# Kernel tuning notes

Measured on AMD Instinct MI355X. Metric: run time of the kernel, lower is better.

Reference implementation:

```python
import jax, jax.numpy as jnp
import numpy as np

B, S, D, N = 8, 2048, 1024, 1024
RMIN, RMAX = 0.9, 0.999
MAX_PHASE = 6.2831853
EPS = 1e-5


def _ln(v):
    # LayerNorm without affine params (elementwise_affine=False)
    mu = jnp.mean(v, axis=-1, keepdims=True)
    var = jnp.var(v, axis=-1, keepdims=True)
    return (v - mu) * jax.lax.rsqrt(var + EPS)


def setup_inputs() -> dict:
    key = jax.random.key(0)
    ks = jax.random.split(key, 12)
    x = jax.random.normal(ks[0], (B, S, D), dtype=jnp.float32)
    hidden_re = jnp.zeros((B, N), dtype=jnp.float32)
    hidden_im = jnp.zeros((B, N), dtype=jnp.float32)
    # LRU ring initialization (Orvieto et al. 2023)
    u1 = jax.random.uniform(ks[1], (N,), dtype=jnp.float32)
    u2 = jax.random.uniform(ks[2], (N,), dtype=jnp.float32)
    nu_log = jnp.log(-0.5 * jnp.log(u1 * (RMAX**2 - RMIN**2) + RMIN**2))
    theta_log = jnp.log(MAX_PHASE * u2)
    B_re = jax.random.normal(ks[3], (N, D), dtype=jnp.float32) / np.sqrt(2 * D)
    B_im = jax.random.normal(ks[4], (N, D), dtype=jnp.float32) / np.sqrt(2 * D)
    C_re = jax.random.normal(ks[5], (N, N), dtype=jnp.float32) / np.sqrt(N)
    C_im = jax.random.normal(ks[6], (N, N), dtype=jnp.float32) / np.sqrt(N)
    D_skip = jax.random.normal(ks[7], (N, D), dtype=jnp.float32) / np.sqrt(D)
    W_gate = jax.random.normal(ks[8], (N, D), dtype=jnp.float32) / np.sqrt(D)  # gating_proj
    W_con = jax.random.normal(ks[9], (D, N), dtype=jnp.float32) / np.sqrt(N)   # contract
    return {"x": x, "hidden_re": hidden_re, "hidden_im": hidden_im,
            "nu_log": nu_log, "theta_log": theta_log,
            "B_re": B_re, "B_im": B_im, "C_re": C_re, "C_im": C_im,
            "D_skip": D_skip, "W_gate": W_gate, "W_con": W_con}


def reference(x, hidden_re, hidden_im, nu_log, theta_log,
              B_re, B_im, C_re, C_im, D_skip, W_gate, W_con):
    residual = x
    # diagonal complex transition lambda and input normalizer gamma
    mag = jnp.exp(-jnp.exp(nu_log))                 # |lambda|, [N]
    phase = jnp.exp(theta_log)
    lam_re = mag * jnp.cos(phase)
    lam_im = mag * jnp.sin(phase)
    gamma = jnp.sqrt(1.0 - mag * mag)               # sqrt(1-|lambda|^2)
    # input projection (complex), pre-scaled by gamma: [B,S,N]
    u_re = jnp.einsum("bsd,nd->bsn", x, B_re) * gamma
    u_im = jnp.einsum("bsd,nd->bsn", x, B_im) * gamma
    # sequential linear recurrence h_t = lambda * h_{t-1} + u_t (complex)
    def step(h, u):
        h_re, h_im = h
        ur, ui = u
        nr = lam_re * h_re - lam_im * h_im + ur
        ni = lam_re * h_im + lam_im * h_re + ui
        return (nr, ni), (nr, ni)
    (hf_re, hf_im), (hs_re, hs_im) = jax.lax.scan(
        step, (hidden_re, hidden_im),
        (jnp.swapaxes(u_re, 0, 1), jnp.swapaxes(u_im, 0, 1)))  # time-major [S,B,N]
    hs_re = jnp.swapaxes(hs_re, 0, 1)  # [B,S,N]
    hs_im = jnp.swapaxes(hs_im, 0, 1)
    # y = Re(C h) + D x
    y = (jnp.einsum("bsn,mn->bsm", hs_re, C_re)
         - jnp.einsum("bsn,mn->bsm", hs_im, C_im)
         + jnp.einsum("bsd,md->bsm", x, D_skip))
    # gated norm / MLP fusion
    y = _ln(y)                                              # rnn_post_norm
    gate = jax.nn.gelu(_ln(jnp.einsum("bsd,nd->bsn", residual, W_gate)), approximate=False)
    y = y * gate
    y = jax.nn.gelu(_ln(y), approximate=False)              # contract_norm + activation
    out = jnp.einsum("bsn,dn->bsd", y, W_con)               # contract
    return (out, hf_re, hf_im)
```

## Files before the change

kernel.cpp:

```cpp
#include <hip/hip_runtime.h>
#include <math.h>

#define Bsz 8
#define Ssz 2048
#define Dsz 1024
#define Nsz 1024
#define CHUNKS 64
#define CLEN 32
#define Msz (Bsz * Ssz)

typedef unsigned short u16;
typedef __attribute__((ext_vector_type(8))) short short8;
typedef __attribute__((ext_vector_type(4))) float floatx4;

__device__ __forceinline__ float b2f(u16 u) {
    unsigned v = ((unsigned)u) << 16; float f; __builtin_memcpy(&f, &v, 4); return f;
}
__device__ __forceinline__ u16 f2b(float f) {
    unsigned u; __builtin_memcpy(&u, &f, 4);
    unsigned r = u + 0x7fffu + ((u >> 16) & 1u);
    return (u16)(r >> 16);
}

__global__ void cvt_kernel(const float* __restrict__ in, u16* __restrict__ out, int n4, float scale) {
    int i = blockIdx.x * blockDim.x + threadIdx.x;
    if (i < n4) {
        float4 v = ((const float4*)in)[i];
        ushort4 o;
        o.x = f2b(v.x * scale); o.y = f2b(v.y * scale);
        o.z = f2b(v.z * scale); o.w = f2b(v.w * scale);
        ((ushort4*)out)[i] = o;
    }
}

__global__ void lam_setup(const float* __restrict__ nu_log, const float* __restrict__ theta_log,
                          float* lam_re, float* lam_im, float* gam,
                          float* lamL_re, float* lamL_im) {
    int n = blockIdx.x * 256 + threadIdx.x;
    if (n >= Nsz) return;
    float mag = expf(-expf(nu_log[n]));
    float ph  = expf(theta_log[n]);
    float lr = mag * cosf(ph), li = mag * sinf(ph);
    lam_re[n] = lr; lam_im[n] = li;
    gam[n] = sqrtf(fmaxf(1.0f - mag * mag, 0.0f));
    float ar = lr, ai = li;
    #pragma unroll
    for (int i = 0; i < 5; ++i) { float nr = ar*ar - ai*ai; float ni = 2.0f*ar*ai; ar = nr; ai = ni; }
    lamL_re[n] = ar; lamL_im[n] = ai;
}

#define BM 128
#define BN 128
#define BK 32

struct GemmJob {
    const u16* A0; const u16* W0;
    const u16* A1; const u16* W1;
    const u16* A2; const u16* W2;
    int P;
    float* outF;
    u16*   outB;
    const float* colscale;
};
struct GemmBatch { GemmJob j[3]; };

__global__ __launch_bounds__(256, 2)
void gemm_bt(GemmBatch batch, int M, int N, int K) {
    const GemmJob job = batch.j[blockIdx.z];
    __shared__ u16 As[BM * BK];
    __shared__ u16 Ws[BN * BK];
    const int tid  = threadIdx.x;
    const int wave = tid >> 6, lane = tid & 63;
    const int bm = blockIdx.x, bn = blockIdx.y;
    const int wm = (wave >> 1) * 64, wn = (wave & 1) * 64;

    floatx4 acc[4][4];
    #pragma unroll
    for (int i = 0; i < 4; ++i)
        #pragma unroll
        for (int j = 0; j < 4; ++j) acc[i][j] = (floatx4){0.f, 0.f, 0.f, 0.f};

    const u16* Aps[3] = { job.A0, job.A1, job.A2 };
    const u16* Wps[3] = { job.W0, job.W1, job.W2 };

    const int srow = wave * 32 + (lane >> 2);
    const int scol = (((lane & 3) ^ ((lane >> 3) & 3))) * 8;
    const int frow = lane & 15;
    const int fk   = (((lane >> 4) ^ ((frow >> 1) & 3))) * 8;

    for (int p = 0; p < job.P; ++p) {
        const u16* A = Aps[p];
        const u16* W = Wps[p];
        const u16* gAb = A + (size_t)(bm * BM + srow) * K + scol;
        const u16* gWb = W + (size_t)(bn * BN + srow) * K + scol;
        for (int kk = 0; kk < K; kk += BK) {
            __syncthreads();
            #pragma unroll
            for (int jj = 0; jj < 2; ++jj) {
                const u16* gA = gAb + (size_t)(jj * 16) * K + kk;
                const u16* gW = gWb + (size_t)(jj * 16) * K + kk;
                u16* lA = As + (wave * 32 + jj * 16) * BK;
                u16* lW = Ws + (wave * 32 + jj * 16) * BK;
                __builtin_amdgcn_global_load_lds((const __attribute__((address_space(1))) void*)gA,
                                                 (__attribute__((address_space(3))) void*)lA, 16, 0, 0);
                __builtin_amdgcn_global_load_lds((const __attribute__((address_space(1))) void*)gW,
                                                 (__attribute__((address_space(3))) void*)lW, 16, 0, 0);
            }
            __syncthreads();
            short8 af[4], wf[4];
            #pragma unroll
            for (int i = 0; i < 4; ++i)
                af[i] = *(const short8*)(As + (wm + i * 16 + frow) * BK + fk);
            #pragma unroll
            for (int i = 0; i < 4; ++i)
                wf[i] = *(const short8*)(Ws + (wn + i * 16 + frow) * BK + fk);
            #pragma unroll
            for (int mi = 0; mi < 4; ++mi)
                #pragma unroll
                for (int ni = 0; ni < 4; ++ni)
                    acc[mi][ni] = __builtin_amdgcn_mfma_f32_16x16x32_bf16(af[mi], wf[ni], acc[mi][ni], 0, 0, 0);
        }
    }

    const int rgrp = lane >> 4;
    const int ccol = lane & 15;
    #pragma unroll
    for (int mi = 0; mi < 4; ++mi) {
        #pragma unroll
        for (int r = 0; r < 4; ++r) {
            int row = bm * BM + wm + mi * 16 + rgrp * 4 + r;
            #pragma unroll
            for (int ni = 0; ni < 4; ++ni) {
                int col = bn * BN + wn + ni * 16 + ccol;
                float v = acc[mi][ni][r];
                if (job.colscale) v *= job.colscale[col];
                size_t idx = (size_t)row * N + col;
                if (job.outF) job.outF[idx] = v;
                else          job.outB[idx] = f2b(v);
            }
        }
    }
}

__global__ void scan_phase1(const u16* __restrict__ u_re, const u16* __restrict__ u_im,
                            const float* __restrict__ lam_re, const float* __restrict__ lam_im,
                            float* __restrict__ carry_re, float* __restrict__ carry_im) {
    int n = blockIdx.x * 256 + threadIdx.x;
    int c = blockIdx.y, b = blockIdx.z;
    float lr = lam_re[n], li = lam_im[n];
    size_t base = ((size_t)b * Ssz + (size_t)c * CLEN) * Nsz + n;
    float hr = 0.f, hi = 0.f;
    #pragma unroll
    for (int t = 0; t < CLEN; ++t) {
        float ur = b2f(u_re[base + (size_t)t * Nsz]);
        float ui = b2f(u_im[base + (size_t)t * Nsz]);
        float nr = fmaf(lr, hr, fmaf(-li, hi, ur));
        float ni = fmaf(lr, hi, fmaf( li, hr, ui));
        hr = nr; hi = ni;
    }
    size_t ci = ((size_t)b * CHUNKS + c) * Nsz + n;
    carry_re[ci] = hr; carry_im[ci] = hi;
}

__global__ void scan_phase2(const float* __restrict__ carry_re, const float* __restrict__ carry_im,
                            const float* __restrict__ lamL_re, const float* __restrict__ lamL_im,
                            const float* __restrict__ hid_re, const float* __restrict__ hid_im,
                            float* __restrict__ entry_re, float* __restrict__ entry_im,
                            float* __restrict__ out_base) {
    int n = blockIdx.x * 256 + threadIdx.x;
    int b = blockIdx.y;
    float Lr = lamL_re[n], Li = lamL_im[n];
    float Hr = hid_re[b * Nsz + n], Hi = hid_im[b * Nsz + n];
    for (int c = 0; c < CHUNKS; ++c) {
        size_t ci = ((size_t)b * CHUNKS + c) * Nsz + n;
        entry_re[ci] = Hr; entry_im[ci] = Hi;
        float cr = carry_re[ci], cim = carry_im[ci];
        float nr = fmaf(Lr, Hr, fmaf(-Li, Hi, cr));
        float ni = fmaf(Lr, Hi, fmaf( Li, Hr, cim));
        Hr = nr; Hi = ni;
    }
    out_base[(size_t)16777216 + (size_t)b * Nsz + n] = Hr;
    out_base[(size_t)16777216 + 8192 + (size_t)b * Nsz + n] = Hi;
}

__global__ void scan_phase3(const u16* __restrict__ u_re, const u16* __restrict__ u_im,
                            const float* __restrict__ lam_re, const float* __restrict__ lam_im,
                            const float* __restrict__ entry_re, const float* __restrict__ entry_im,
                            u16* __restrict__ hs_re, u16* __restrict__ hs_im) {
    int n = blockIdx.x * 256 + threadIdx.x;
    int c = blockIdx.y, b = blockIdx.z;
    float lr = lam_re[n], li = lam_im[n];
    size_t ci = ((size_t)b * CHUNKS + c) * Nsz + n;
    float hr = entry_re[ci], hi = entry_im[ci];
    size_t base = ((size_t)b * Ssz + (size_t)c * CLEN) * Nsz + n;
    #pragma unroll
    for (int t = 0; t < CLEN; ++t) {
        float ur = b2f(u_re[base + (size_t)t * Nsz]);
        float ui = b2f(u_im[base + (size_t)t * Nsz]);
        float nr = fmaf(lr, hr, fmaf(-li, hi, ur));
        float ni = fmaf(lr, hi, fmaf( li, hr, ui));
        hr = nr; hi = ni;
        hs_re[base + (size_t)t * Nsz] = f2b(hr);
        hs_im[base + (size_t)t * Nsz] = f2b(hi);
    }
}

__device__ __forceinline__ float waveReduce(float v) {
    #pragma unroll
    for (int off = 32; off > 0; off >>= 1) v += __shfl_down(v, off, 64);
    return v;
}
__device__ __forceinline__ float gelu_exact(float x) {
    return 0.5f * x * (1.0f + erff(x * 0.70710678118654752f));
}

__global__ __launch_bounds__(256)
void fuse_ln(const u16* __restrict__ y_raw, const u16* __restrict__ gate_pre, u16* __restrict__ y3) {
    int row = blockIdx.x;
    int tid = threadIdx.x;
    int wave = tid >> 6, lane = tid & 63;
    size_t base = (size_t)row * Nsz + tid * 4;
    ushort4 yv = *(const ushort4*)(y_raw + base);
    ushort4 gv = *(const ushort4*)(gate_pre + base);
    float y[4] = { b2f(yv.x), b2f(yv.y), b2f(yv.z), b2f(yv.w) };
    float g[4] = { b2f(gv.x), b2f(gv.y), b2f(gv.z), b2f(gv.w) };

    float sy = 0.f, sy2 = 0.f, sg = 0.f, sg2 = 0.f;
    #pragma unroll
    for (int i = 0; i < 4; ++i) {
        sy += y[i]; sy2 += y[i] * y[i];
        sg += g[i]; sg2 += g[i] * g[i];
    }
    __shared__ float sh[16];
    sy = waveReduce(sy); sy2 = waveReduce(sy2);
    sg = waveReduce(sg); sg2 = waveReduce(sg2);
    if (lane == 0) { sh[wave] = sy; sh[wave + 4] = sy2; sh[wave + 8] = sg; sh[wave + 12] = sg2; }
    __syncthreads();
    sy  = sh[0] + sh[1] + sh[2] + sh[3];
    sy2 = sh[4] + sh[5] + sh[6] + sh[7];
    sg  = sh[8] + sh[9] + sh[10] + sh[11];
    sg2 = sh[12] + sh[13] + sh[14] + sh[15];
    const float inv = 1.0f / (float)Nsz;
    float muy = sy * inv, vary = sy2 * inv - muy * muy, ry = rsqrtf(vary + 1e-5f);
    float mug = sg * inv, varg = sg2 * inv - mug * mug, rg = rsqrtf(varg + 1e-5f);

    float y2[4]; float s2 = 0.f, s22 = 0.f;
    #pragma unroll
    for (int i = 0; i < 4; ++i) {
        float ly = (y[i] - muy) * ry;
        float lg = (g[i] - mug) * rg;
        float t = ly * gelu_exact(lg);
        y2[i] = t; s2 += t; s22 += t * t;
    }
    s2 = waveReduce(s2); s22 = waveReduce(s22);
    __syncthreads();
    if (lane == 0) { sh[wave] = s2; sh[wave + 4] = s22; }
    __syncthreads();
    s2  = sh[0] + sh[1] + sh[2] + sh[3];
    s22 = sh[4] + sh[5] + sh[6] + sh[7];
    float mu2 = s2 * inv, var2 = s22 * inv - mu2 * mu2, r2 = rsqrtf(var2 + 1e-5f);
    ushort4 ov;
    ov.x = f2b(gelu_exact((y2[0] - mu2) * r2));
    ov.y = f2b(gelu_exact((y2[1] - mu2) * r2));
    ov.z = f2b(gelu_exact((y2[2] - mu2) * r2));
    ov.w = f2b(gelu_exact((y2[3] - mu2) * r2));
    *(ushort4*)(y3 + base) = ov;
}

extern "C" void kernel_launch(void* const* d_in, const int* in_sizes, int n_in,
                              void* d_out, int out_size, void* d_ws, size_t ws_size,
                              hipStream_t stream) {
    const float* x         = (const float*)d_in[0];
    const float* hid_re    = (const float*)d_in[1];
    const float* hid_im    = (const float*)d_in[2];
    const float* nu_log    = (const float*)d_in[3];
    const float* theta_log = (const float*)d_in[4];
    const float* B_re      = (const float*)d_in[5];
    const float* B_im      = (const float*)d_in[6];
    const float* C_re      = (const float*)d_in[7];
    const float* C_im      = (const float*)d_in[8];
    const float* D_skip    = (const float*)d_in[9];
    const float* W_gate    = (const float*)d_in[10];
    const float* W_con     = (const float*)d_in[11];
    float* out = (float*)d_out;

    char* ws = (char*)d_ws;
    const size_t MB = 1ull << 20;
    u16* wBre  = (u16*)(ws + 0 * MB);
    u16* wBim  = (u16*)(ws + 2 * MB);
    u16* wCre  = (u16*)(ws + 4 * MB);
    u16* wCimN = (u16*)(ws + 6 * MB);
    u16* wDsk  = (u16*)(ws + 8 * MB);
    u16* wWg   = (u16*)(ws + 10 * MB);
    u16* wWc   = (u16*)(ws + 12 * MB);
    float* lam_re = (float*)(ws + 14 * MB);
    float* lam_im = lam_re + 1024;
    float* gam    = lam_re + 2048;
    float* lamLre = lam_re + 3072;
    float* lamLim = lam_re + 4096;
    u16* xb    = (u16*)(ws + 16 * MB);
    u16* u_re  = (u16*)(ws + 48 * MB);
    u16* u_im  = (u16*)(ws + 80 * MB);
    u16* gate  = (u16*)(ws + 112 * MB);
    u16* hs_re = (u16*)(ws + 144 * MB);
    u16* hs_im = (u16*)(ws + 176 * MB);
    float* carry_re = (float*)(ws + 208 * MB);
    float* carry_im = (float*)(ws + 210 * MB);
    float* entry_re = (float*)(ws + 212 * MB);
    float* entry_im = (float*)(ws + 214 * MB);
    u16* y_raw = u_re;
    u16* y3    = u_im;

    cvt_kernel<<<16384, 256, 0, stream>>>(x, xb, (Msz * Dsz) / 4, 1.0f);
    cvt_kernel<<<1024, 256, 0, stream>>>(B_re,   wBre,  (Nsz * Dsz) / 4, 1.0f);
    cvt_kernel<<<1024, 256, 0, stream>>>(B_im,   wBim,  (Nsz * Dsz) / 4, 1.0f);
    cvt_kernel<<<1024, 256, 0, stream>>>(C_re,   wCre,  (Nsz * Nsz) / 4, 1.0f);
    cvt_kernel<<<1024, 256, 0, stream>>>(C_im,   wCimN, (Nsz * Nsz) / 4, -1.0f);
    cvt_kernel<<<1024, 256, 0, stream>>>(D_skip, wDsk,  (Nsz * Dsz) / 4, 1.0f);
    cvt_kernel<<<1024, 256, 0, stream>>>(W_gate, wWg,   (Nsz * Dsz) / 4, 1.0f);
    cvt_kernel<<<1024, 256, 0, stream>>>(W_con,  wWc,   (Dsz * Nsz) / 4, 1.0f);
    lam_setup<<<4, 256, 0, stream>>>(nu_log, theta_log, lam_re, lam_im, gam, lamLre, lamLim);

    GemmBatch b1 = {};
    b1.j[0] = { xb, wBre, nullptr, nullptr, nullptr, nullptr, 1, nullptr, u_re, gam };
    b1.j[1] = { xb, wBim, nullptr, nullptr, nullptr, nullptr, 1, nullptr, u_im, gam };
    b1.j[2] = { xb, wWg,  nullptr, nullptr, nullptr, nullptr, 1, nullptr, gate, nullptr };
    gemm_bt<<<dim3(Msz / BM, Nsz / BN, 3), 256, 0, stream>>>(b1, Msz, Nsz, Dsz);

    scan_phase1<<<dim3(Nsz / 256, CHUNKS, Bsz), 256, 0, stream>>>(u_re, u_im, lam_re, lam_im, carry_re, carry_im);
    scan_phase2<<<dim3(Nsz / 256, Bsz), 256, 0, stream>>>(carry_re, carry_im, lamLre, lamLim,
                                                          hid_re, hid_im, entry_re, entry_im, out);
    scan_phase3<<<dim3(Nsz / 256, CHUNKS, Bsz), 256, 0, stream>>>(u_re, u_im, lam_re, lam_im,
                                                                  entry_re, entry_im, hs_re, hs_im);

    GemmBatch b2 = {};
    b2.j[0] = { hs_re, wCre, hs_im, wCimN, xb, wDsk, 3, nullptr, y_raw, nullptr };
    gemm_bt<<<dim3(Msz / BM, Nsz / BN, 1), 256, 0, stream>>>(b2, Msz, Nsz, Nsz);

    fuse_ln<<<Msz, 256, 0, stream>>>(y_raw, gate, y3);

    GemmBatch b3 = {};
    b3.j[0] = { y3, wWc, nullptr, nullptr, nullptr, nullptr, 1, out, nullptr, nullptr };
    gemm_bt<<<dim3(Msz / BM, Dsz / BN, 1), 256, 0, stream>>>(b3, Msz, Dsz, Nsz);

    (void)in_sizes; (void)n_in; (void)out_size; (void)ws_size;
}
```

Measured before the change: 527.7 us.

## Double GEMM K-tile to 64 with new LDS swizzle and batch conversions

Raises the GEMM K tile from 32 to 64 and reworks the global-to-LDS load pattern and XOR swizzle to match, so each barrier pair now covers two MFMA sub-steps. This halves the number of synchronisations and loop iterations per K sweep. Shared memory per block doubles, which may limit how many blocks fit per CU. Separately, the eight fp32-to-bf16 conversion launches are merged into one kernel that picks its job from a block-offset table, removing launch overhead.

```diff
diff --git a/kernel.cpp b/kernel.cpp
--- a/kernel.cpp
+++ b/kernel.cpp
@@ -22,14 +22,28 @@
     return (u16)(r >> 16);
 }
 
-__global__ void cvt_kernel(const float* __restrict__ in, u16* __restrict__ out, int n4, float scale) {
-    int i = blockIdx.x * blockDim.x + threadIdx.x;
-    if (i < n4) {
-        float4 v = ((const float4*)in)[i];
+struct CvtJobs {
+    const float* src[8];
+    u16* dst[8];
+    int n4[8];
+    float scale[8];
+    int blk_start[9];
+};
+
+__global__ __launch_bounds__(256)
+void cvt_multi(CvtJobs J) {
+    int b = blockIdx.x;
+    int j = 0;
+    #pragma unroll
+    for (int t = 0; t < 7; ++t) if (b >= J.blk_start[t + 1]) j = t + 1;
+    int i = (b - J.blk_start[j]) * 256 + threadIdx.x;
+    if (i < J.n4[j]) {
+        float4 v = ((const float4*)J.src[j])[i];
+        float s = J.scale[j];
         ushort4 o;
-        o.x = f2b(v.x * scale); o.y = f2b(v.y * scale);
-        o.z = f2b(v.z * scale); o.w = f2b(v.w * scale);
-        ((ushort4*)out)[i] = o;
+        o.x = f2b(v.x * s); o.y = f2b(v.y * s);
+        o.z = f2b(v.z * s); o.w = f2b(v.w * s);
+        ((ushort4*)J.dst[j])[i] = o;
     }
 }
 
@@ -51,7 +65,7 @@
 
 #define BM 128
 #define BN 128
-#define BK 32
+#define BK 64
 
 struct GemmJob {
     const u16* A0; const u16* W0;
@@ -83,42 +97,48 @@
     const u16* Aps[3] = { job.A0, job.A1, job.A2 };
     const u16* Wps[3] = { job.W0, job.W1, job.W2 };
 
-    const int srow = wave * 32 + (lane >> 2);
-    const int scol = (((lane & 3) ^ ((lane >> 3) & 3))) * 8;
+    const int srow8 = lane >> 3;
+    const int scol  = ((lane & 7) ^ srow8) * 8;
     const int frow = lane & 15;
-    const int fk   = (((lane >> 4) ^ ((frow >> 1) & 3))) * 8;
+    const int fq   = lane >> 4;
+    const int fsw  = frow & 7;
 
     for (int p = 0; p < job.P; ++p) {
         const u16* A = Aps[p];
         const u16* W = Wps[p];
-        const u16* gAb = A + (size_t)(bm * BM + srow) * K + scol;
-        const u16* gWb = W + (size_t)(bn * BN + srow) * K + scol;
+        const u16* gAb = A + (size_t)(bm * BM + srow8) * K + scol;
+        const u16* gWb = W + (size_t)(bn * BN + srow8) * K + scol;
         for (int kk = 0; kk < K; kk += BK) {
             __syncthreads();
             #pragma unroll
-            for (int jj = 0; jj < 2; ++jj) {
-                const u16* gA = gAb + (size_t)(jj * 16) * K + kk;
-                const u16* gW = gWb + (size_t)(jj * 16) * K + kk;
-                u16* lA = As + (wave * 32 + jj * 16) * BK;
-                u16* lW = Ws + (wave * 32 + jj * 16) * BK;
+            for (int jj = 0; jj < 4; ++jj) {
+                const int row0 = wave * 32 + jj * 8;
+                const u16* gA = gAb + (size_t)row0 * K + kk;
+                const u16* gW = gWb + (size_t)row0 * K + kk;
+                u16* lA = As + row0 * BK;
+                u16* lW = Ws + row0 * BK;
                 __builtin_amdgcn_global_load_lds((const __attribute__((address_space(1))) void*)gA,
                                                  (__attribute__((address_space(3))) void*)lA, 16, 0, 0);
                 __builtin_amdgcn_global_load_lds((const __attribute__((address_space(1))) void*)gW,
                                                  (__attribute__((address_space(3))) void*)lW, 16, 0, 0);
             }
             __syncthreads();
-            short8 af[4], wf[4];
             #pragma unroll
-            for (int i = 0; i < 4; ++i)
-                af[i] = *(const short8*)(As + (wm + i * 16 + frow) * BK + fk);
-            #pragma unroll
-            for (int i = 0; i < 4; ++i)
-                wf[i] = *(const short8*)(Ws + (wn + i * 16 + frow) * BK + fk);
-            #pragma unroll
-            for (int mi = 0; mi < 4; ++mi)
+            for (int h = 0; h < 2; ++h) {
+                const int ca = ((h << 2) | fq) ^ fsw;
+                short8 af[4], wf[4];
                 #pragma unroll
-                for (int ni = 0; ni < 4; ++ni)
-                    acc[mi][ni] = __builtin_amdgcn_mfma_f32_16x16x32_bf16(af[mi], wf[ni], acc[mi][ni], 0, 0, 0);
+                for (int i = 0; i < 4; ++i)
+                    af[i] = *(const short8*)(As + (wm + i * 16 + frow) * BK + ca * 8);
+                #pragma unroll
+                for (int i = 0; i < 4; ++i)
+                    wf[i] = *(const short8*)(Ws + (wn + i * 16 + frow) * BK + ca * 8);
+                #pragma unroll
+                for (int mi = 0; mi < 4; ++mi)
+                    #pragma unroll
+                    for (int ni = 0; ni < 4; ++ni)
+                        acc[mi][ni] = __builtin_amdgcn_mfma_f32_16x16x32_bf16(af[mi], wf[ni], acc[mi][ni], 0, 0, 0);
+            }
         }
     }
 
@@ -311,14 +331,21 @@
     u16* y_raw = u_re;
     u16* y3    = u_im;
 
-    cvt_kernel<<<16384, 256, 0, stream>>>(x, xb, (Msz * Dsz) / 4, 1.0f);
-    cvt_kernel<<<1024, 256, 0, stream>>>(B_re,   wBre,  (Nsz * Dsz) / 4, 1.0f);
-    cvt_kernel<<<1024, 256, 0, stream>>>(B_im,   wBim,  (Nsz * Dsz) / 4, 1.0f);
-    cvt_kernel<<<1024, 256, 0, stream>>>(C_re,   wCre,  (Nsz * Nsz) / 4, 1.0f);
-    cvt_kernel<<<1024, 256, 0, stream>>>(C_im,   wCimN, (Nsz * Nsz) / 4, -1.0f);
-    cvt_kernel<<<1024, 256, 0, stream>>>(D_skip, wDsk,  (Nsz * Dsz) / 4, 1.0f);
-    cvt_kernel<<<1024, 256, 0, stream>>>(W_gate, wWg,   (Nsz * Dsz) / 4, 1.0f);
-    cvt_kernel<<<1024, 256, 0, stream>>>(W_con,  wWc,   (Dsz * Nsz) / 4, 1.0f);
+    CvtJobs J = {};
+    const int WQ = (Nsz * Dsz) / 4;
+    const int WB = WQ / 256;
+    J.src[0] = x;      J.dst[0] = xb;    J.n4[0] = (Msz * Dsz) / 4; J.scale[0] = 1.0f;
+    J.src[1] = B_re;   J.dst[1] = wBre;  J.n4[1] = WQ; J.scale[1] = 1.0f;
+    J.src[2] = B_im;   J.dst[2] = wBim;  J.n4[2] = WQ; J.scale[2] = 1.0f;
+    J.src[3] = C_re;   J.dst[3] = wCre;  J.n4[3] = WQ; J.scale[3] = 1.0f;
+    J.src[4] = C_im;   J.dst[4] = wCimN; J.n4[4] = WQ; J.scale[4] = -1.0f;
+    J.src[5] = D_skip; J.dst[5] = wDsk;  J.n4[5] = WQ; J.scale[5] = 1.0f;
+    J.src[6] = W_gate; J.dst[6] = wWg;   J.n4[6] = WQ; J.scale[6] = 1.0f;
+    J.src[7] = W_con;  J.dst[7] = wWc;   J.n4[7] = WQ; J.scale[7] = 1.0f;
+    J.blk_start[0] = 0;
+    J.blk_start[1] = 16384;
+    for (int t = 2; t <= 8; ++t) J.blk_start[t] = J.blk_start[t - 1] + WB;
+    cvt_multi<<<J.blk_start[8], 256, 0, stream>>>(J);
     lam_setup<<<4, 256, 0, stream>>>(nu_log, theta_log, lam_re, lam_im, gam, lamLre, lamLim);
 
     GemmBatch b1 = {};
```

Result: faster. 505.0 us (-4.3%).
